# Optimization experiments

Measured on AMD Instinct MI355X. Metric: run time of the kernel, lower is better.

## Reference

```python
import jax, jax.numpy as jnp
import numpy as np

N_NODES = 100000
N_EDGES = 1600000
C = 64          # in = hidden = out channels
L = 3           # num_layers
BN_EPS = 1e-5


def setup_inputs() -> dict:
    key = jax.random.key(0)
    ks = jax.random.split(key, 16)
    x = jax.random.normal(ks[0], (N_NODES, C), dtype=jnp.float32)
    edge_index = jax.random.randint(ks[1], (2, N_EDGES), 0, N_NODES, dtype=jnp.int32)
    s = 1.0 / np.sqrt(C)
    # Stacked per-layer parameters (all layers are C->C).
    # Linear weights stored as [in, out] (i.e. torch weight transposed).
    W1 = jax.random.normal(ks[2], (L, C, C), dtype=jnp.float32) * s
    b1 = jnp.zeros((L, C), dtype=jnp.float32)
    g1 = jnp.ones((L, C), dtype=jnp.float32)    # MLP BN1 gamma
    be1 = jnp.zeros((L, C), dtype=jnp.float32)  # MLP BN1 beta
    W2 = jax.random.normal(ks[3], (L, C, C), dtype=jnp.float32) * s
    b2 = jnp.zeros((L, C), dtype=jnp.float32)
    g2 = jnp.ones((L, C), dtype=jnp.float32)
    be2 = jnp.zeros((L, C), dtype=jnp.float32)
    bn_g = jnp.ones((L, C), dtype=jnp.float32)   # outer per-layer BN gamma
    bn_be = jnp.zeros((L, C), dtype=jnp.float32)
    eps = jnp.zeros((L,), dtype=jnp.float32)     # GIN eps per layer
    return {"x": x, "edge_index": edge_index, "eps": eps,
            "W1": W1, "b1": b1, "g1": g1, "be1": be1,
            "W2": W2, "b2": b2, "g2": g2, "be2": be2,
            "bn_g": bn_g, "bn_be": bn_be}


def _bn(h, g, b):
    # Inference-mode BatchNorm1d with running_mean=0, running_var=1.
    return g * (h * (1.0 / np.sqrt(1.0 + BN_EPS))) + b


def reference(x, edge_index, eps, W1, b1, g1, be1, W2, b2, g2, be2, bn_g, bn_be):
    src, dst = edge_index[0], edge_index[1]
    for i in range(L):
        # GIN message passing: gather source features, scatter-add to targets.
        agg = jax.ops.segment_sum(x[src], dst, num_segments=N_NODES)  # [N, C]
        h = (1.0 + eps[i]) * x + agg
        # 2-layer MLP: Linear -> BN -> ReLU, twice.
        h = jax.nn.relu(_bn(h @ W1[i] + b1[i], g1[i], be1[i]))
        h = jax.nn.relu(_bn(h @ W2[i] + b2[i], g2[i], be2[i]))
        # Outer per-layer BatchNorm.
        x = _bn(h, bn_g[i], bn_be[i])
        if i < L - 1:
            x = jax.nn.relu(x)  # dropout is identity in eval mode
    return x
```

## Files before the change

### kernel.cpp

```cpp
#include <hip/hip_runtime.h>
#include <hip/hip_fp16.h>

#define N_NODES 100000
#define N_EDGES 1600000
#define CH 64
#define NLAYERS 3
#define NF2 784
#define SLABF 2560
#define NPART 1000
#define EPB2 1600

typedef _Float16 half8 __attribute__((ext_vector_type(8)));
typedef float floatx4 __attribute__((ext_vector_type(4)));

static __device__ __forceinline__ float4 ld4(const float* p){ return *(const float4*)p; }
static __device__ __forceinline__ unsigned pack2(float a, float b){
  __half2 h = __float22half2_rn(make_float2(a, b));
  return *(unsigned*)&h;
}
static __device__ __forceinline__ half8 ldh8(const unsigned short* p){
  uint4 u = *(const uint4*)p;
  return *(half8*)&u;
}

__global__ __launch_bounds__(256) void part12_kernel(const int* __restrict__ src, const int* __restrict__ dst,
                                                     int* __restrict__ ftail, int* __restrict__ pairs2,
                                                     const float* __restrict__ x, unsigned short* __restrict__ xb){
  __shared__ int hist[NF2];
  __shared__ int cur[NF2];
  int tid = threadIdx.x;
  for (int i = tid; i < NF2; i += 256) hist[i] = 0;
  __syncthreads();
  int base = blockIdx.x * EPB2;
  int eend = base + EPB2;
  for (int e = base + tid; e < eend; e += 256) {
    atomicAdd(&hist[dst[e] >> 7], 1);
  }
  __syncthreads();
  for (int i = tid; i < NF2; i += 256) {
    int c = hist[i];
    cur[i] = c ? atomicAdd(&ftail[i], c) : 0;
  }
  __syncthreads();
  for (int e = base + tid; e < eend; e += 256) {
    int s = src[e], d = dst[e];
    int f = d >> 7;
    int idx = atomicAdd(&cur[f], 1);
    if (idx < (f+1)*SLABF)
      pairs2[idx] = s | ((d & 127) << 20);
  }
  for (int i = (blockIdx.x*256 + tid)*8; i < N_NODES*CH; i += NPART*256*8) {
    float4 v0 = ld4(x + i), v1 = ld4(x + i + 4);
    uint4 w;
    w.x = pack2(v0.x, v0.y); w.y = pack2(v0.z, v0.w);
    w.z = pack2(v1.x, v1.y); w.w = pack2(v1.z, v1.w);
    *(uint4*)(xb + i) = w;
  }
}

__global__ __launch_bounds__(256) void csr_kernel(const int* __restrict__ pairs2, const int* __restrict__ ftail,
                                                  int* __restrict__ offs, int* __restrict__ offe,
                                                  int* __restrict__ srclist){
  __shared__ int c[128];
  __shared__ int s[128];
  __shared__ int cur[128];
  int t = threadIdx.x;
  int f = blockIdx.x;
  int e0 = f*SLABF;
  int e1 = ftail[f]; int emax = e0 + SLABF; if (e1 > emax) e1 = emax;
  if (t < 128) c[t] = 0;
  __syncthreads();
  for (int i = e0 + t; i < e1; i += 256) {
    int p = pairs2[i];
    atomicAdd(&c[((unsigned)p >> 20) & 127], 1);
  }
  __syncthreads();
  int v = (t < 128) ? c[t] : 0;
  if (t < 128) s[t] = v;
  __syncthreads();
  #pragma unroll
  for (int o = 1; o < 128; o <<= 1){
    int u = 0;
    if (t < 128 && t >= o) u = s[t-o];
    __syncthreads();
    if (t < 128) s[t] += u;
    __syncthreads();
  }
  if (t < 128) {
    int excl = s[t] - v;
    cur[t] = excl;
    int n = f*128 + t;
    if (n < N_NODES) { offs[n] = e0 + excl; offe[n] = e0 + excl + v; }
  }
  __syncthreads();
  for (int i = e0 + t; i < e1; i += 256) {
    int p = pairs2[i];
    int pos = atomicAdd(&cur[((unsigned)p >> 20) & 127], 1);
    if (pos < SLABF)
      srclist[e0 + pos] = p & 0xFFFFF;
  }
}

__global__ __launch_bounds__(256) void prep_kernel(
    const float* __restrict__ W1, const float* __restrict__ b1,
    const float* __restrict__ g1, const float* __restrict__ be1,
    const float* __restrict__ W2, const float* __restrict__ b2,
    const float* __restrict__ g2, const float* __restrict__ be2,
    const float* __restrict__ bng, const float* __restrict__ bnb,
    _Float16* __restrict__ Wt, float* __restrict__ bf, float* __restrict__ ogb,
    int* __restrict__ ftail){
  const float s = 0.9999950000374997f;
  int i = blockIdx.x*256 + threadIdx.x;
  if (i < NF2) ftail[i] = i*SLABF;
  if (i < NLAYERS*4096) {
    int l = i >> 12, rem = i & 4095, k = rem >> 6, n = rem & 63;
    int di = n*64 + (((k>>3) ^ (n&7))<<3) + (k&7);
    Wt[l*8192 + di]        = (_Float16)(W1[i] * g1[l*64+n] * s);
    Wt[l*8192 + 4096 + di] = (_Float16)(W2[i] * g2[l*64+n] * s);
  }
  if (i < NLAYERS*64) {
    int l = i >> 6, j = i & 63;
    bf[l*128 + j]      = b1[i]*g1[i]*s + be1[i];
    bf[l*128 + 64 + j] = b2[i]*g2[i]*s + be2[i];
    ogb[i]                 = bng[i]*s;
    ogb[NLAYERS*64 + i]    = bnb[i];
  }
}

__global__ __launch_bounds__(256, 8) void layer_kernel(const unsigned short* __restrict__ XBin,
                                                    const int* __restrict__ offs, const int* __restrict__ offe,
                                                    const int* __restrict__ srclist,
                                                    const float* __restrict__ eps,
                                                    const _Float16* __restrict__ Wt,
                                                    const float* __restrict__ bf, const float* __restrict__ ogb,
                                                    int layer, float* __restrict__ outf,
                                                    _Float16* __restrict__ outb, int relu_out){
  __shared__ _Float16 HsA[64*64];
  __shared__ _Float16 Wts[64*64];
  int tid = threadIdx.x;
  int b = blockIdx.x;
  const _Float16* Wg = Wt + layer*8192;
  *(uint4*)&Wts[tid*8]       = *(const uint4*)&Wg[tid*8];
  *(uint4*)&Wts[(tid+256)*8] = *(const uint4*)&Wg[(tid+256)*8];

  float ep = 1.0f + eps[layer];
  int kb = tid & 7;
  const unsigned short* xr = XBin + (kb << 3);
  #pragma unroll
  for (int p = 0; p < 2; ++p) {
    int nl = p*32 + (tid >> 3);
    int n = b*64 + nl;
    float r[8] = {0,0,0,0,0,0,0,0};
    if (n < N_NODES) {
      half8 A = (half8)(_Float16)0, B = A, C = A, D = A, E = A, F = A, G = A, H = A;
      int e0 = offs[n], e1 = offe[n];
      int e = e0;
      if (e + 8 <= e1) {
        half8 u0 = ldh8(xr + (srclist[e  ]<<6));
        half8 u1 = ldh8(xr + (srclist[e+1]<<6));
        half8 u2 = ldh8(xr + (srclist[e+2]<<6));
        half8 u3 = ldh8(xr + (srclist[e+3]<<6));
        half8 u4 = ldh8(xr + (srclist[e+4]<<6));
        half8 u5 = ldh8(xr + (srclist[e+5]<<6));
        half8 u6 = ldh8(xr + (srclist[e+6]<<6));
        half8 u7 = ldh8(xr + (srclist[e+7]<<6));
        e += 8;
        for (; e + 8 <= e1; e += 8) {
          half8 v0 = ldh8(xr + (srclist[e  ]<<6));
          half8 v1 = ldh8(xr + (srclist[e+1]<<6));
          half8 v2 = ldh8(xr + (srclist[e+2]<<6));
          half8 v3 = ldh8(xr + (srclist[e+3]<<6));
          half8 v4 = ldh8(xr + (srclist[e+4]<<6));
          half8 v5 = ldh8(xr + (srclist[e+5]<<6));
          half8 v6 = ldh8(xr + (srclist[e+6]<<6));
          half8 v7 = ldh8(xr + (srclist[e+7]<<6));
          A += u0; B += u1; C += u2; D += u3;
          E += u4; F += u5; G += u6; H += u7;
          u0 = v0; u1 = v1; u2 = v2; u3 = v3;
          u4 = v4; u5 = v5; u6 = v6; u7 = v7;
        }
        A += u0; B += u1; C += u2; D += u3;
        E += u4; F += u5; G += u6; H += u7;
      }
      for (; e+4 <= e1; e += 4) {
        half8 u0 = ldh8(xr + (srclist[e  ]<<6));
        half8 u1 = ldh8(xr + (srclist[e+1]<<6));
        half8 u2 = ldh8(xr + (srclist[e+2]<<6));
        half8 u3 = ldh8(xr + (srclist[e+3]<<6));
        A += u0; B += u1; C += u2; D += u3;
      }
      for (; e < e1; ++e) {
        A += ldh8(xr + (srclist[e]<<6));
      }
      half8 S = ((A + B) + (C + D)) + ((E + F) + (G + H));
      half8 sv = ldh8(xr + (n<<6));
      #pragma unroll
      for (int i = 0; i < 8; ++i) r[i] = fmaf(ep, (float)sv[i], (float)S[i]);
    }
    uint4 w;
    w.x = pack2(r[0], r[1]); w.y = pack2(r[2], r[3]);
    w.z = pack2(r[4], r[5]); w.w = pack2(r[6], r[7]);
    *(uint4*)&HsA[nl*64 + ((kb ^ (nl&7))<<3)] = w;
  }
  __syncthreads();

  int lane = tid & 63;
  int wid = tid >> 6;
  int c = lane & 15;
  int q = lane >> 4;
  int mbase = wid*16;
  int ma = mbase + c;

  half8 a0 = *(const half8*)&HsA[ma*64 + (((q)   ^ (ma&7))<<3)];
  half8 a1 = *(const half8*)&HsA[ma*64 + (((4+q) ^ (ma&7))<<3)];

  floatx4 acc[4];
  #pragma unroll
  for (int nt = 0; nt < 4; ++nt) {
    int n = nt*16 + c;
    float bv = bf[layer*128 + n];
    floatx4 Acc = {bv, bv, bv, bv};
    half8 b0 = *(const half8*)&Wts[n*64 + (((q)   ^ (n&7))<<3)];
    half8 b1 = *(const half8*)&Wts[n*64 + (((4+q) ^ (n&7))<<3)];
    Acc = __builtin_amdgcn_mfma_f32_16x16x32_f16(a0, b0, Acc, 0, 0, 0);
    Acc = __builtin_amdgcn_mfma_f32_16x16x32_f16(a1, b1, Acc, 0, 0, 0);
    acc[nt] = Acc;
  }
  __syncthreads();

  #pragma unroll
  for (int nt = 0; nt < 4; ++nt) {
    int n = nt*16 + c;
    #pragma unroll
    for (int r = 0; r < 4; ++r) {
      int m = mbase + q*4 + r;
      float h = acc[nt][r]; h = h > 0.f ? h : 0.f;
      HsA[m*64 + (((n>>3) ^ (m&7))<<3) + (n&7)] = (_Float16)h;
    }
  }
  *(uint4*)&Wts[tid*8]       = *(const uint4*)&Wg[4096 + tid*8];
  *(uint4*)&Wts[(tid+256)*8] = *(const uint4*)&Wg[4096 + (tid+256)*8];
  __syncthreads();

  half8 c0 = *(const half8*)&HsA[ma*64 + (((q)   ^ (ma&7))<<3)];
  half8 c1 = *(const half8*)&HsA[ma*64 + (((4+q) ^ (ma&7))<<3)];
  floatx4 acc2[4];
  #pragma unroll
  for (int nt = 0; nt < 4; ++nt) {
    int n = nt*16 + c;
    float bv = bf[layer*128 + 64 + n];
    floatx4 Acc = {bv, bv, bv, bv};
    half8 b0 = *(const half8*)&Wts[n*64 + (((q)   ^ (n&7))<<3)];
    half8 b1 = *(const half8*)&Wts[n*64 + (((4+q) ^ (n&7))<<3)];
    Acc = __builtin_amdgcn_mfma_f32_16x16x32_f16(c0, b0, Acc, 0, 0, 0);
    Acc = __builtin_amdgcn_mfma_f32_16x16x32_f16(c1, b1, Acc, 0, 0, 0);
    acc2[nt] = Acc;
  }

  #pragma unroll
  for (int nt = 0; nt < 4; ++nt) {
    int n = nt*16 + c;
    float og = ogb[layer*64 + n];
    float ob = ogb[NLAYERS*64 + layer*64 + n];
    #pragma unroll
    for (int r = 0; r < 4; ++r) {
      int m = mbase + q*4 + r;
      int gnode = b*64 + m;
      if (gnode < N_NODES) {
        float h = acc2[nt][r]; h = h > 0.f ? h : 0.f;
        float o = fmaf(og, h, ob);
        if (relu_out) {
          o = o > 0.f ? o : 0.f;
          outb[(size_t)gnode*CH + n] = (_Float16)o;
        } else {
          outf[(size_t)gnode*CH + n] = o;
        }
      }
    }
  }
}

extern "C" void kernel_launch(void* const* d_in, const int* in_sizes, int n_in,
                              void* d_out, int out_size, void* d_ws, size_t ws_size,
                              hipStream_t stream) {
  const float* x0  = (const float*)d_in[0];
  const int*   ei  = (const int*)d_in[1];
  const float* eps = (const float*)d_in[2];
  const float* W1  = (const float*)d_in[3];
  const float* b1  = (const float*)d_in[4];
  const float* g1  = (const float*)d_in[5];
  const float* be1 = (const float*)d_in[6];
  const float* W2  = (const float*)d_in[7];
  const float* b2  = (const float*)d_in[8];
  const float* g2  = (const float*)d_in[9];
  const float* be2 = (const float*)d_in[10];
  const float* bng = (const float*)d_in[11];
  const float* bnb = (const float*)d_in[12];
  const int* src = ei;
  const int* dst = ei + N_EDGES;
  float* OUT = (float*)d_out;

  char* p = (char*)d_ws;
  auto carve = [&](size_t bytes)->char*{ char* r = p; p += (bytes + 255) & ~(size_t)255; return r; };
  int*   offs    = (int*)carve((size_t)N_NODES*sizeof(int));
  int*   offe    = (int*)carve((size_t)N_NODES*sizeof(int));
  int*   ftail   = (int*)carve(NF2*sizeof(int));
  int*   pairs2  = (int*)carve((size_t)NF2*SLABF*sizeof(int));
  int*   srclist = (int*)carve((size_t)NF2*SLABF*sizeof(int));
  unsigned short* XB0 = (unsigned short*)carve((size_t)N_NODES*CH*2);
  unsigned short* XB1 = (unsigned short*)carve((size_t)N_NODES*CH*2);
  _Float16* Wt   = (_Float16*)carve((size_t)NLAYERS*2*4096*2);
  float* bfb     = (float*)carve((size_t)NLAYERS*2*64*sizeof(float));
  float* ogb     = (float*)carve((size_t)2*NLAYERS*64*sizeof(float));

  prep_kernel<<<48, 256, 0, stream>>>(W1,b1,g1,be1,W2,b2,g2,be2,bng,bnb,Wt,bfb,ogb,ftail);
  part12_kernel<<<NPART, 256, 0, stream>>>(src, dst, ftail, pairs2, x0, XB0);
  csr_kernel<<<NF2, 256, 0, stream>>>(pairs2, ftail, offs, offe, srclist);

  const int nlb = (N_NODES + 63)/64;
  layer_kernel<<<nlb, 256, 0, stream>>>(XB0, offs, offe, srclist, eps, Wt, bfb, ogb, 0, OUT, (_Float16*)XB1, 1);
  layer_kernel<<<nlb, 256, 0, stream>>>(XB1, offs, offe, srclist, eps, Wt, bfb, ogb, 1, OUT, (_Float16*)XB0, 1);
  layer_kernel<<<nlb, 256, 0, stream>>>(XB0, offs, offe, srclist, eps, Wt, bfb, ogb, 2, OUT, (_Float16*)XB1, 0);
}
```

Baseline: 281.1 us.

## Replace slab-based two-pass CSR build with global histogram, scan, scatter

```diff
diff --git a/kernel.cpp b/kernel.cpp
--- a/kernel.cpp
+++ b/kernel.cpp
@@ -5,10 +5,8 @@
 #define N_EDGES 1600000
 #define CH 64
 #define NLAYERS 3
-#define NF2 784
-#define SLABF 2560
-#define NPART 1000
-#define EPB2 1600
+#define CHK 98
+#define HG 1024
 
 typedef _Float16 half8 __attribute__((ext_vector_type(8)));
 typedef float floatx4 __attribute__((ext_vector_type(4)));
@@ -21,84 +19,6 @@
 static __device__ __forceinline__ half8 ldh8(const unsigned short* p){
   uint4 u = *(const uint4*)p;
   return *(half8*)&u;
-}
-
-__global__ __launch_bounds__(256) void part12_kernel(const int* __restrict__ src, const int* __restrict__ dst,
-                                                     int* __restrict__ ftail, int* __restrict__ pairs2,
-                                                     const float* __restrict__ x, unsigned short* __restrict__ xb){
-  __shared__ int hist[NF2];
-  __shared__ int cur[NF2];
-  int tid = threadIdx.x;
-  for (int i = tid; i < NF2; i += 256) hist[i] = 0;
-  __syncthreads();
-  int base = blockIdx.x * EPB2;
-  int eend = base + EPB2;
-  for (int e = base + tid; e < eend; e += 256) {
-    atomicAdd(&hist[dst[e] >> 7], 1);
-  }
-  __syncthreads();
-  for (int i = tid; i < NF2; i += 256) {
-    int c = hist[i];
-    cur[i] = c ? atomicAdd(&ftail[i], c) : 0;
-  }
-  __syncthreads();
-  for (int e = base + tid; e < eend; e += 256) {
-    int s = src[e], d = dst[e];
-    int f = d >> 7;
-    int idx = atomicAdd(&cur[f], 1);
-    if (idx < (f+1)*SLABF)
-      pairs2[idx] = s | ((d & 127) << 20);
-  }
-  for (int i = (blockIdx.x*256 + tid)*8; i < N_NODES*CH; i += NPART*256*8) {
-    float4 v0 = ld4(x + i), v1 = ld4(x + i + 4);
-    uint4 w;
-    w.x = pack2(v0.x, v0.y); w.y = pack2(v0.z, v0.w);
-    w.z = pack2(v1.x, v1.y); w.w = pack2(v1.z, v1.w);
-    *(uint4*)(xb + i) = w;
-  }
-}
-
-__global__ __launch_bounds__(256) void csr_kernel(const int* __restrict__ pairs2, const int* __restrict__ ftail,
-                                                  int* __restrict__ offs, int* __restrict__ offe,
-                                                  int* __restrict__ srclist){
-  __shared__ int c[128];
-  __shared__ int s[128];
-  __shared__ int cur[128];
-  int t = threadIdx.x;
-  int f = blockIdx.x;
-  int e0 = f*SLABF;
-  int e1 = ftail[f]; int emax = e0 + SLABF; if (e1 > emax) e1 = emax;
-  if (t < 128) c[t] = 0;
-  __syncthreads();
-  for (int i = e0 + t; i < e1; i += 256) {
-    int p = pairs2[i];
-    atomicAdd(&c[((unsigned)p >> 20) & 127], 1);
-  }
-  __syncthreads();
-  int v = (t < 128) ? c[t] : 0;
-  if (t < 128) s[t] = v;
-  __syncthreads();
-  #pragma unroll
-  for (int o = 1; o < 128; o <<= 1){
-    int u = 0;
-    if (t < 128 && t >= o) u = s[t-o];
-    __syncthreads();
-    if (t < 128) s[t] += u;
-    __syncthreads();
-  }
-  if (t < 128) {
-    int excl = s[t] - v;
-    cur[t] = excl;
-    int n = f*128 + t;
-    if (n < N_NODES) { offs[n] = e0 + excl; offe[n] = e0 + excl + v; }
-  }
-  __syncthreads();
-  for (int i = e0 + t; i < e1; i += 256) {
-    int p = pairs2[i];
-    int pos = atomicAdd(&cur[((unsigned)p >> 20) & 127], 1);
-    if (pos < SLABF)
-      srclist[e0 + pos] = p & 0xFFFFF;
-  }
 }
 
 __global__ __launch_bounds__(256) void prep_kernel(
@@ -108,10 +28,10 @@
     const float* __restrict__ g2, const float* __restrict__ be2,
     const float* __restrict__ bng, const float* __restrict__ bnb,
     _Float16* __restrict__ Wt, float* __restrict__ bf, float* __restrict__ ogb,
-    int* __restrict__ ftail){
+    int* __restrict__ deg){
   const float s = 0.9999950000374997f;
   int i = blockIdx.x*256 + threadIdx.x;
-  if (i < NF2) ftail[i] = i*SLABF;
+  if (i < N_NODES) deg[i] = 0;
   if (i < NLAYERS*4096) {
     int l = i >> 12, rem = i & 4095, k = rem >> 6, n = rem & 63;
     int di = n*64 + (((k>>3) ^ (n&7))<<3) + (k&7);
@@ -124,6 +44,63 @@
     bf[l*128 + 64 + j] = b2[i]*g2[i]*s + be2[i];
     ogb[i]                 = bng[i]*s;
     ogb[NLAYERS*64 + i]    = bnb[i];
+  }
+}
+
+__global__ __launch_bounds__(256) void hist_kernel(const int* __restrict__ dst, int* __restrict__ deg,
+                                                   const float* __restrict__ x, unsigned short* __restrict__ xb){
+  int t0 = blockIdx.x*256 + threadIdx.x;
+  for (int e = t0; e < N_EDGES; e += HG*256)
+    atomicAdd(&deg[dst[e]], 1);
+  for (int i = t0*8; i < N_NODES*CH; i += HG*256*8) {
+    float4 v0 = ld4(x + i), v1 = ld4(x + i + 4);
+    uint4 w;
+    w.x = pack2(v0.x, v0.y); w.y = pack2(v0.z, v0.w);
+    w.z = pack2(v1.x, v1.y); w.w = pack2(v1.z, v1.w);
+    *(uint4*)(xb + i) = w;
+  }
+}
+
+__global__ __launch_bounds__(1024) void scan_kernel(const int* __restrict__ deg,
+                                                    int* __restrict__ offs, int* __restrict__ offe,
+                                                    int* __restrict__ cursor){
+  __shared__ int ps[1024];
+  int t = threadIdx.x;
+  int cs = t*CHK;
+  int sum = 0;
+  #pragma unroll 7
+  for (int j = 0; j < CHK; ++j) {
+    int n = cs + j;
+    if (n < N_NODES) sum += deg[n];
+  }
+  ps[t] = sum;
+  __syncthreads();
+  #pragma unroll
+  for (int o = 1; o < 1024; o <<= 1) {
+    int u = (t >= o) ? ps[t-o] : 0;
+    __syncthreads();
+    ps[t] += u;
+    __syncthreads();
+  }
+  int run = ps[t] - sum;
+  for (int j = 0; j < CHK; ++j) {
+    int n = cs + j;
+    if (n < N_NODES) {
+      int d = deg[n];
+      offs[n] = run; cursor[n] = run; offe[n] = run + d;
+      run += d;
+    }
+  }
+}
+
+__global__ __launch_bounds__(256) void scatter_kernel(const int* __restrict__ src, const int* __restrict__ dst,
+                                                      int* __restrict__ cursor, int* __restrict__ srclist){
+  int t0 = blockIdx.x*256 + threadIdx.x;
+  for (int e = t0; e < N_EDGES; e += HG*256) {
+    int s = src[e], d = dst[e];
+    int pos = atomicAdd(&cursor[d], 1);
+    if (pos < N_EDGES)
+      srclist[pos] = s;
   }
 }
 
@@ -302,20 +279,21 @@
 
   char* p = (char*)d_ws;
   auto carve = [&](size_t bytes)->char*{ char* r = p; p += (bytes + 255) & ~(size_t)255; return r; };
+  int*   deg     = (int*)carve((size_t)N_NODES*sizeof(int));
   int*   offs    = (int*)carve((size_t)N_NODES*sizeof(int));
   int*   offe    = (int*)carve((size_t)N_NODES*sizeof(int));
-  int*   ftail   = (int*)carve(NF2*sizeof(int));
-  int*   pairs2  = (int*)carve((size_t)NF2*SLABF*sizeof(int));
-  int*   srclist = (int*)carve((size_t)NF2*SLABF*sizeof(int));
+  int*   cursor  = (int*)carve((size_t)N_NODES*sizeof(int));
+  int*   srclist = (int*)carve((size_t)N_EDGES*sizeof(int));
   unsigned short* XB0 = (unsigned short*)carve((size_t)N_NODES*CH*2);
   unsigned short* XB1 = (unsigned short*)carve((size_t)N_NODES*CH*2);
   _Float16* Wt   = (_Float16*)carve((size_t)NLAYERS*2*4096*2);
   float* bfb     = (float*)carve((size_t)NLAYERS*2*64*sizeof(float));
   float* ogb     = (float*)carve((size_t)2*NLAYERS*64*sizeof(float));
 
-  prep_kernel<<<48, 256, 0, stream>>>(W1,b1,g1,be1,W2,b2,g2,be2,bng,bnb,Wt,bfb,ogb,ftail);
-  part12_kernel<<<NPART, 256, 0, stream>>>(src, dst, ftail, pairs2, x0, XB0);
-  csr_kernel<<<NF2, 256, 0, stream>>>(pairs2, ftail, offs, offe, srclist);
+  prep_kernel<<<(N_NODES + 255)/256, 256, 0, stream>>>(W1,b1,g1,be1,W2,b2,g2,be2,bng,bnb,Wt,bfb,ogb,deg);
+  hist_kernel<<<HG, 256, 0, stream>>>(dst, deg, x0, XB0);
+  scan_kernel<<<1, 1024, 0, stream>>>(deg, offs, offe, cursor);
+  scatter_kernel<<<HG, 256, 0, stream>>>(src, dst, cursor, srclist);
 
   const int nlb = (N_NODES + 63)/64;
   layer_kernel<<<nlb, 256, 0, stream>>>(XB0, offs, offe, srclist, eps, Wt, bfb, ogb, 0, OUT, (_Float16*)XB1, 1);
```

New measurement: 704.3 us. +150.6%, slower.
